# Performance work log

Measured on AMD Instinct MI355X. Metric: run time of the kernel, lower is better.

## Reference

```python
import jax, jax.numpy as jnp
import numpy as np

HEADS = 4
SCALE = 10.0
DIM = 128
VOL = (16, 16, 16)
BATCH = 2
EPS = 1e-12  # F.normalize eps


def setup_inputs() -> dict:
    key = jax.random.key(0)
    ks = jax.random.split(key, 7)
    h, w, z = VOL
    shape = (BATCH, DIM, h, w, z)
    wstd = 1.0 / np.sqrt(DIM)
    return {
        "x": jax.random.normal(ks[0], shape, dtype=jnp.float32),
        "cond_x": jax.random.normal(ks[1], shape, dtype=jnp.float32),
        "Wq": jax.random.normal(ks[2], (DIM, DIM), dtype=jnp.float32) * wstd,
        "bq": jnp.zeros((DIM,), dtype=jnp.float32),
        "Wk": jax.random.normal(ks[3], (DIM, DIM), dtype=jnp.float32) * wstd,
        "bk": jnp.zeros((DIM,), dtype=jnp.float32),
        "Wv": jax.random.normal(ks[4], (DIM, DIM), dtype=jnp.float32) * wstd,
        "bv": jnp.zeros((DIM,), dtype=jnp.float32),
        "Wo": jax.random.normal(ks[5], (DIM, DIM), dtype=jnp.float32) * wstd,
        "bo": jnp.zeros((DIM,), dtype=jnp.float32),
    }


def _l2norm_last(t):
    # F.normalize(t, dim=-1): divide by max(||t||_2, eps) along last axis
    n = jnp.sqrt(jnp.sum(t * t, axis=-1, keepdims=True))
    return t / jnp.maximum(n, EPS)


def reference(x, cond_x, Wq, bq, Wk, bk, Wv, bv, Wo, bo):
    b, c, h, w, z = x.shape
    N = h * w * z
    d = c // HEADS
    xf = x.reshape(b, c, N)          # conv1x1 == per-voxel linear over channels
    cf = cond_x.reshape(b, c, N)
    q = jnp.einsum('oc,bcn->bon', Wq, xf) + bq[None, :, None]
    k = jnp.einsum('oc,bcn->bon', Wk, cf) + bk[None, :, None]
    v = jnp.einsum('oc,bcn->bon', Wv, cf) + bv[None, :, None]
    # 'b (h c) n -> b h c n'
    q = q.reshape(b, HEADS, d, N)
    k = k.reshape(b, HEADS, d, N)
    v = v.reshape(b, HEADS, d, N)
    # NOTE: original normalizes dim=-1 of [b,h,d,N] -> over the SPATIAL axis
    q = _l2norm_last(q)
    k = _l2norm_last(k)
    sim = jnp.einsum('bhdi,bhdj->bhij', q, k) * SCALE   # [b,h,N,N]
    attn = jax.nn.softmax(sim, axis=-1)
    out = jnp.einsum('bhij,bhdj->bhid', attn, v)        # [b,h,N,d]
    # 'b h n d -> b (h d) n' then back to volume
    out = out.transpose(0, 1, 3, 2).reshape(b, c, N)
    out = jnp.einsum('oc,bcn->bon', Wo, out) + bo[None, :, None]
    return out.reshape(b, c, h, w, z)
```

## Files before the change

kernel.cpp:

```cpp
#include <hip/hip_runtime.h>
#include <hip/hip_bf16.h>
#include <math.h>

#define NSP 4096
#define CD 128
#define NB 2
#define NH 4
#define JS 4
#define JSTEP 64
#define NSTEP ((NSP / JS) / JSTEP)

typedef __attribute__((ext_vector_type(8))) short bf16x8;
typedef __attribute__((ext_vector_type(4))) float f32x4;

static constexpr float QSCALE = 10.0f * 1.4426950408889634f;

__device__ __forceinline__ ushort f2bf(float f) {
    union { float f; unsigned u; } v; v.f = f;
    unsigned r = v.u + 0x7fffu + ((v.u >> 16) & 1u);
    return (ushort)(r >> 16);
}
__device__ __forceinline__ float bf2f(ushort u) {
    union { unsigned u; float f; } v; v.u = ((unsigned)u) << 16;
    return v.f;
}
__device__ __forceinline__ unsigned pk2bf(float a, float b) {
    union { __hip_bfloat162 h; unsigned u; } t;
    t.h = __float22bfloat162_rn(make_float2(a, b));
    return t.u;
}
__device__ __forceinline__ void gload_lds16(const void* g, void* l) {
    __builtin_amdgcn_global_load_lds(
        (const __attribute__((address_space(1))) unsigned int*)g,
        (__attribute__((address_space(3))) unsigned int*)l, 16, 0, 0);
}

__global__ __launch_bounds__(256) void cast_all(
    const float* __restrict__ x, const float* __restrict__ cx,
    const float* __restrict__ Wq, const float* __restrict__ Wk,
    const float* __restrict__ Wv, const float* __restrict__ Wo,
    ushort* __restrict__ Xt, ushort* __restrict__ Ct, ushort* __restrict__ Wall)
{
    const int t = threadIdx.x;
    if (blockIdx.x >= 128) {
        const int sub = blockIdx.x - 128;
        const int m = blockIdx.z * 2 + blockIdx.y;
        const float* src = (m == 0) ? Wq : (m == 1) ? Wk : (m == 2) ? Wv : Wo;
        const int off = sub * 1024 + t * 4;
        const float4 v = *(const float4*)(src + off);
        ushort4 o;
        o.x = f2bf(v.x); o.y = f2bf(v.y); o.z = f2bf(v.z); o.w = f2bf(v.w);
        *(ushort4*)(Wall + m * 16384 + off) = o;
        return;
    }
    __shared__ ushort L[32][130];
    const int n0 = blockIdx.x * 32;
    const int b  = blockIdx.y;
    const float* in = (blockIdx.z == 0) ? x : cx;
    ushort* outp    = (blockIdx.z == 0) ? Xt : Ct;
    const int nl = t & 31, cq = t >> 5;
    #pragma unroll
    for (int cc = cq; cc < CD; cc += 8)
        L[nl][cc] = f2bf(in[((size_t)b * CD + cc) * NSP + n0 + nl]);
    __syncthreads();
    const int nr = t >> 3, cs = (t & 7) * 16;
    unsigned u[8];
    #pragma unroll
    for (int w = 0; w < 8; ++w)
        u[w] = (unsigned)L[nr][cs + 2 * w] | ((unsigned)L[nr][cs + 2 * w + 1] << 16);
    ushort* dst = outp + ((size_t)(b * NSP + n0 + nr)) * CD + cs;
    *(uint4*)(dst)     = make_uint4(u[0], u[1], u[2], u[3]);
    *(uint4*)(dst + 8) = make_uint4(u[4], u[5], u[6], u[7]);
}

__global__ __launch_bounds__(256) void proj_qkv_mfma(
    const ushort* __restrict__ Xt, const ushort* __restrict__ Ct,
    const ushort* __restrict__ Wall,
    const float* __restrict__ Bq, const float* __restrict__ Bk, const float* __restrict__ Bv,
    ushort* __restrict__ qh, ushort* __restrict__ kh, ushort* __restrict__ V16,
    float* __restrict__ partQ, float* __restrict__ partK)
{
    const int t = threadIdx.x;
    const int wid = t >> 6, lane = t & 63;
    const int g = lane >> 4, n16 = lane & 15;
    const int nt = blockIdx.x;
    const int b  = nt >> 8;
    const int xblk = nt & 255;
    const int nb = xblk * 16;
    const int o0 = (blockIdx.y * 4 + wid) * 16;

    const ushort* Wq = Wall;
    const ushort* Wk = Wall + 16384;
    const ushort* Wv = Wall + 32768;
    const size_t xrow = ((size_t)(b * NSP + nb + n16)) * CD;
    const size_t wrow = (size_t)(o0 + n16) * CD;

    f32x4 aq = {0,0,0,0}, ak = {0,0,0,0}, av = {0,0,0,0};
    #pragma unroll
    for (int ks = 0; ks < 4; ++ks) {
        const int k0 = ks * 32 + g * 8;
        const bf16x8 bx = *(const bf16x8*)(Xt + xrow + k0);
        const bf16x8 bc = *(const bf16x8*)(Ct + xrow + k0);
        const bf16x8 wqf = *(const bf16x8*)(Wq + wrow + k0);
        const bf16x8 wkf = *(const bf16x8*)(Wk + wrow + k0);
        const bf16x8 wvf = *(const bf16x8*)(Wv + wrow + k0);
        aq = __builtin_amdgcn_mfma_f32_16x16x32_bf16(wqf, bx, aq, 0, 0, 0);
        ak = __builtin_amdgcn_mfma_f32_16x16x32_bf16(wkf, bc, ak, 0, 0, 0);
        av = __builtin_amdgcn_mfma_f32_16x16x32_bf16(wvf, bc, av, 0, 0, 0);
    }
    float sq[4], sk[4];
    #pragma unroll
    for (int r = 0; r < 4; ++r) {
        const int o = o0 + 4 * g + r;
        const size_t row = ((size_t)(b * CD + o)) * NSP + nb + n16;
        const float qv = aq[r] + Bq[o];
        const float kv = ak[r] + Bk[o];
        qh[row]  = f2bf(qv);
        kh[row]  = f2bf(kv);
        V16[row] = f2bf(av[r] + Bv[o]);
        sq[r] = qv * qv; sk[r] = kv * kv;
    }
    #pragma unroll
    for (int r = 0; r < 4; ++r) {
        #pragma unroll
        for (int off = 1; off < 16; off <<= 1) {
            sq[r] += __shfl_xor(sq[r], off);
            sk[r] += __shfl_xor(sk[r], off);
        }
    }
    if (n16 == 0) {
        #pragma unroll
        for (int r = 0; r < 4; ++r) {
            const int ch = b * CD + o0 + 4 * g + r;
            partQ[(size_t)ch * 256 + xblk] = sq[r];
            partK[(size_t)ch * 256 + xblk] = sk[r];
        }
    }
}

__global__ __launch_bounds__(256) void normfin(
    const float* __restrict__ partQ, const float* __restrict__ partK,
    float* __restrict__ scq, float* __restrict__ sck)
{
    const int ch = blockIdx.x & 255, isK = blockIdx.x >> 8;
    const float* p = (isK ? partK : partQ) + (size_t)ch * 256;
    const int t = threadIdx.x;
    float v = p[t];
    #pragma unroll
    for (int off = 32; off > 0; off >>= 1) v += __shfl_down(v, off, 64);
    __shared__ float red[4];
    if ((t & 63) == 0) red[t >> 6] = v;
    __syncthreads();
    if (t == 0) {
        const float total = red[0] + red[1] + red[2] + red[3];
        const float sc = (isK ? 1.0f : QSCALE) / fmaxf(sqrtf(total), 1e-12f);
        (isK ? sck : scq)[ch] = sc;
    }
}

__global__ __launch_bounds__(256) void pack_qk(
    const ushort* __restrict__ qh, const ushort* __restrict__ kh,
    const float* __restrict__ scq, const float* __restrict__ sck,
    ushort* __restrict__ Qt, ushort* __restrict__ Kt)
{
    const int n  = blockIdx.x * 256 + threadIdx.x;
    const int bh = blockIdx.y, cq = blockIdx.z;
    const int b = bh >> 2, h = bh & 3;
    unsigned qw[4], kw[4];
    #pragma unroll
    for (int e = 0; e < 4; ++e) {
        const int dp = cq * 4 + e;
        const int gr = b * CD + h * 32 + 2 * dp;
        const float fq0 = bf2f(qh[(size_t)gr * NSP + n]) * scq[gr];
        const float fq1 = bf2f(qh[(size_t)(gr + 1) * NSP + n]) * scq[gr + 1];
        const float fk0 = bf2f(kh[(size_t)gr * NSP + n]) * sck[gr];
        const float fk1 = bf2f(kh[(size_t)(gr + 1) * NSP + n]) * sck[gr + 1];
        qw[e] = pk2bf(fq0, fq1);
        kw[e] = pk2bf(fk0, fk1);
    }
    const int jb = n >> 6, jr = n & 63;
    const size_t base = ((size_t)(bh * (NSP / 64) + jb)) * 4 + cq;
    *(uint4*)(Qt + base * 512 + jr * 8) = make_uint4(qw[0], qw[1], qw[2], qw[3]);
    *(uint4*)(Kt + base * 512 + jr * 8) = make_uint4(kw[0], kw[1], kw[2], kw[3]);
}

__global__ __launch_bounds__(256, 4) void attn_mfma(
    const ushort* __restrict__ Qt, const ushort* __restrict__ Kt,
    const ushort* __restrict__ V16,
    unsigned* __restrict__ pacc, float* __restrict__ pl)
{
    __shared__ __align__(16) ushort Kl[4][2048];
    __shared__ __align__(16) ushort Vl[4][2048];

    const int t = threadIdx.x;
    const int wid = t >> 6, lane = t & 63;
    const int g = lane >> 4, n16 = lane & 15;
    const int f = blockIdx.x;
    const int bh = f & 7, it32 = (f >> 3) & 31, js = f >> 8;
    const int b = bh >> 2, h = bh & 3;
    const int i0 = it32 * 128 + wid * 32;

    const ushort* QtB = Qt + (size_t)bh * NSP * 32;
    const ushort* KtB = Kt + (size_t)bh * NSP * 32;
    const ushort* Vb  = V16 + (size_t)(b * CD + h * 32) * NSP;

    const size_t qoff = ((size_t)(i0 >> 6) * 4 + g) * 512 + (size_t)(i0 & 63) * 8;
    const bf16x8 qf0 = *(const bf16x8*)(QtB + qoff + n16 * 8);
    const bf16x8 qf1 = *(const bf16x8*)(QtB + qoff + (16 + n16) * 8);

    f32x4 acc00 = {0,0,0,0}, acc01 = {0,0,0,0}, acc10 = {0,0,0,0}, acc11 = {0,0,0,0};
    float l0 = 0.f, l1 = 0.f;
    const f32x4 zero = {0,0,0,0};

    const int klp = lane ^ (wid * 2);
    const int vd  = wid * 8 + (lane >> 3);
    const int vsw = (lane & 7) ^ (lane >> 3);
    auto stageK = [&](int buf, int jt) {
        gload_lds16(KtB + ((size_t)(jt >> 6) * 4 + wid) * 512 + klp * 8,
                    &Kl[buf][wid * 512]);
    };
    auto stageV = [&](int buf, int jt) {
        gload_lds16(Vb + (size_t)vd * NSP + jt + vsw * 8, &Vl[buf][wid * 512]);
    };

    const int jbeg = js * (NSP / JS);
    stageK(0, jbeg);          stageV(0, jbeg);
    stageK(1, jbeg + JSTEP);  stageV(1, jbeg + JSTEP);

    for (int step = 0; step < NSTEP; ++step) {
        const int jt = jbeg + step * JSTEP;
        if (step + 2 < NSTEP) {
            stageK((step + 2) & 3, jt + 2 * JSTEP);
            stageV((step + 2) & 3, jt + 2 * JSTEP);
            asm volatile("s_waitcnt vmcnt(4)" ::: "memory");
        } else if (step + 1 < NSTEP) {
            asm volatile("s_waitcnt vmcnt(2)" ::: "memory");
        } else {
            asm volatile("s_waitcnt vmcnt(0)" ::: "memory");
        }
        __builtin_amdgcn_s_barrier();
        const int cur = step & 3;

        #pragma unroll
        for (int s = 0; s < 2; ++s) {
            const bf16x8 kf0 = *(const bf16x8*)(&Kl[cur][g * 512 + ((s * 32 + n16) ^ (g * 2)) * 8]);
            const bf16x8 kf1 = *(const bf16x8*)(&Kl[cur][g * 512 + ((s * 32 + 16 + n16) ^ (g * 2)) * 8]);
            const int c0 = ((4 * s + (g >> 1)) ^ (n16 & 7)) * 8 + (g & 1) * 4;
            const int c1 = ((4 * s + 2 + (g >> 1)) ^ (n16 & 7)) * 8 + (g & 1) * 4;
            union { uint2 u2[2]; bf16x8 v; } v0, v1;
            v0.u2[0] = *(const uint2*)(&Vl[cur][n16 * 64 + c0]);
            v0.u2[1] = *(const uint2*)(&Vl[cur][n16 * 64 + c1]);
            v1.u2[0] = *(const uint2*)(&Vl[cur][(16 + n16) * 64 + c0]);
            v1.u2[1] = *(const uint2*)(&Vl[cur][(16 + n16) * 64 + c1]);

            #pragma unroll
            for (int it = 0; it < 2; ++it) {
                const bf16x8 qf = it ? qf1 : qf0;
                f32x4 s0 = __builtin_amdgcn_mfma_f32_16x16x32_bf16(kf0, qf, zero, 0, 0, 0);
                f32x4 s1 = __builtin_amdgcn_mfma_f32_16x16x32_bf16(kf1, qf, zero, 0, 0, 0);
                const float p0 = __builtin_amdgcn_exp2f(s0.x);
                const float p1 = __builtin_amdgcn_exp2f(s0.y);
                const float p2 = __builtin_amdgcn_exp2f(s0.z);
                const float p3 = __builtin_amdgcn_exp2f(s0.w);
                const float p4 = __builtin_amdgcn_exp2f(s1.x);
                const float p5 = __builtin_amdgcn_exp2f(s1.y);
                const float p6 = __builtin_amdgcn_exp2f(s1.z);
                const float p7 = __builtin_amdgcn_exp2f(s1.w);
                const float ps = ((p0 + p1) + (p2 + p3)) + ((p4 + p5) + (p6 + p7));
                if (it) l1 += ps; else l0 += ps;
                union { unsigned u[4]; bf16x8 v; } pf;
                pf.u[0] = pk2bf(p0, p1);
                pf.u[1] = pk2bf(p2, p3);
                pf.u[2] = pk2bf(p4, p5);
                pf.u[3] = pk2bf(p6, p7);
                if (it) {
                    acc10 = __builtin_amdgcn_mfma_f32_16x16x32_bf16(v0.v, pf.v, acc10, 0, 0, 0);
                    acc11 = __builtin_amdgcn_mfma_f32_16x16x32_bf16(v1.v, pf.v, acc11, 0, 0, 0);
                } else {
                    acc00 = __builtin_amdgcn_mfma_f32_16x16x32_bf16(v0.v, pf.v, acc00, 0, 0, 0);
                    acc01 = __builtin_amdgcn_mfma_f32_16x16x32_bf16(v1.v, pf.v, acc01, 0, 0, 0);
                }
            }
        }
    }

    l0 += __shfl_xor(l0, 16); l0 += __shfl_xor(l0, 32);
    l1 += __shfl_xor(l1, 16); l1 += __shfl_xor(l1, 32);

    const size_t base = (size_t)js * 8 + bh;
    if (lane < 16) {
        pl[base * NSP + i0 + n16]      = l0;
        pl[base * NSP + i0 + 16 + n16] = l1;
    }
    unsigned* pb = pacc + base * 16 * NSP;
    const int col0 = i0 + n16, col1 = i0 + 16 + n16;
    pb[(size_t)(2 * g)     * NSP + col0] = pk2bf(acc00[0], acc00[1]);
    pb[(size_t)(2 * g + 1) * NSP + col0] = pk2bf(acc00[2], acc00[3]);
    pb[(size_t)(8 + 2 * g)     * NSP + col0] = pk2bf(acc01[0], acc01[1]);
    pb[(size_t)(8 + 2 * g + 1) * NSP + col0] = pk2bf(acc01[2], acc01[3]);
    pb[(size_t)(2 * g)     * NSP + col1] = pk2bf(acc10[0], acc10[1]);
    pb[(size_t)(2 * g + 1) * NSP + col1] = pk2bf(acc10[2], acc10[3]);
    pb[(size_t)(8 + 2 * g)     * NSP + col1] = pk2bf(acc11[0], acc11[1]);
    pb[(size_t)(8 + 2 * g + 1) * NSP + col1] = pk2bf(acc11[2], acc11[3]);
}

__global__ __launch_bounds__(256) void combine_kernel(
    const unsigned* __restrict__ pacc, const float* __restrict__ pl,
    ushort* __restrict__ Yt)
{
    const int i  = blockIdx.x * 256 + threadIdx.x;
    const int bh = blockIdx.y, z = blockIdx.z;
    const int b = bh >> 2, h = bh & 3;
    float L = 0.f;
    #pragma unroll
    for (int s = 0; s < JS; ++s) L += pl[((size_t)(s * 8 + bh)) * NSP + i];
    const float invL = 1.0f / L;
    unsigned u[4];
    #pragma unroll
    for (int e = 0; e < 4; ++e) {
        const int dp = z * 4 + e;
        float a0 = 0.f, a1 = 0.f;
        #pragma unroll
        for (int s = 0; s < JS; ++s) {
            const unsigned w = pacc[(((size_t)(s * 8 + bh)) * 16 + dp) * NSP + i];
            union { unsigned u; float f; } lo, hi;
            lo.u = w << 16; hi.u = w & 0xffff0000u;
            a0 += lo.f; a1 += hi.f;
        }
        u[e] = pk2bf(a0 * invL, a1 * invL);
    }
    ushort* dst = Yt + ((size_t)(b * NSP + i)) * CD + h * 32 + z * 8;
    *(uint4*)(dst) = make_uint4(u[0], u[1], u[2], u[3]);
}

__global__ __launch_bounds__(256) void proj_out_mfma(
    const ushort* __restrict__ Yt, const ushort* __restrict__ Wall,
    const float* __restrict__ Bo, float* __restrict__ outp)
{
    const int t = threadIdx.x;
    const int wid = t >> 6, lane = t & 63;
    const int g = lane >> 4, n16 = lane & 15;
    const int nt = blockIdx.x;
    const int b  = nt >> 8;
    const int nb = (nt & 255) * 16;
    const int o0 = (blockIdx.y * 4 + wid) * 16;

    const ushort* Wo = Wall + 49152;
    const size_t xrow = ((size_t)(b * NSP + nb + n16)) * CD;
    const size_t wrow = (size_t)(o0 + n16) * CD;

    f32x4 a = {0,0,0,0};
    #pragma unroll
    for (int ks = 0; ks < 4; ++ks) {
        const int k0 = ks * 32 + g * 8;
        const bf16x8 bx = *(const bf16x8*)(Yt + xrow + k0);
        const bf16x8 wf = *(const bf16x8*)(Wo + wrow + k0);
        a = __builtin_amdgcn_mfma_f32_16x16x32_bf16(wf, bx, a, 0, 0, 0);
    }
    #pragma unroll
    for (int r = 0; r < 4; ++r) {
        const int o = o0 + 4 * g + r;
        outp[((size_t)(b * CD + o)) * NSP + nb + n16] = a[r] + Bo[o];
    }
}

extern "C" void kernel_launch(void* const* d_in, const int* in_sizes, int n_in,
                              void* d_out, int out_size, void* d_ws, size_t ws_size,
                              hipStream_t stream)
{
    const float* x  = (const float*)d_in[0];
    const float* cx = (const float*)d_in[1];
    const float* Wq = (const float*)d_in[2];
    const float* bq = (const float*)d_in[3];
    const float* Wk = (const float*)d_in[4];
    const float* bk = (const float*)d_in[5];
    const float* Wv = (const float*)d_in[6];
    const float* bv = (const float*)d_in[7];
    const float* Wo = (const float*)d_in[8];
    const float* bo = (const float*)d_in[9];
    float* out = (float*)d_out;

    char* w = (char*)d_ws;
    ushort*  qh   = (ushort*)w;  w += (size_t)NB * CD * NSP * 2;
    ushort*  kh   = (ushort*)w;  w += (size_t)NB * CD * NSP * 2;
    float*   scq  = (float*)w;   w += 1024;
    float*   sck  = (float*)w;   w += 1024;
    float*   partQ = (float*)w;  w += (size_t)NB * CD * 256 * 4;
    float*   partK = (float*)w;  w += (size_t)NB * CD * 256 * 4;
    ushort*  Qt   = (ushort*)w;  w += (size_t)NB * NH * NSP * 32 * 2;
    ushort*  Kt   = (ushort*)w;  w += (size_t)NB * NH * NSP * 32 * 2;
    ushort*  V16  = (ushort*)w;  w += (size_t)NB * CD * NSP * 2;
    unsigned* pacc = (unsigned*)w; w += (size_t)JS * 8 * 16 * NSP * 4;
    float*   pl   = (float*)w;   w += (size_t)JS * 8 * NSP * 4;
    ushort*  Xt   = (ushort*)w;  w += (size_t)NB * NSP * CD * 2;
    ushort*  Ct   = (ushort*)w;  w += (size_t)NB * NSP * CD * 2;
    ushort*  Yt   = (ushort*)w;  w += (size_t)NB * NSP * CD * 2;
    ushort*  Wall = (ushort*)w;

    cast_all<<<dim3(144, NB, 2), 256, 0, stream>>>(x, cx, Wq, Wk, Wv, Wo, Xt, Ct, Wall);
    proj_qkv_mfma<<<dim3(512, 2), 256, 0, stream>>>(Xt, Ct, Wall, bq, bk, bv,
                                                    qh, kh, V16, partQ, partK);
    normfin<<<dim3(512), 256, 0, stream>>>(partQ, partK, scq, sck);
    pack_qk<<<dim3(16, 8, 4), 256, 0, stream>>>(qh, kh, scq, sck, Qt, Kt);
    attn_mfma<<<dim3(1024), 256, 0, stream>>>(Qt, Kt, V16, pacc, pl);
    combine_kernel<<<dim3(16, 8, 4), 256, 0, stream>>>(pacc, pl, Yt);
    proj_out_mfma<<<dim3(512, 2), 256, 0, stream>>>(Yt, Wall, bo, out);
}
```

Measured before the change: 72.90 us.

## Fold Q/K normalization into attention, drop pack kernel, fuse combine with output projection

The QKV projection now writes unnormalized Q and K straight into the tiled layout the attention kernel reads, so the separate pack_qk pass and the qh/kh intermediates go away. The Q and K norms are merged into one per-channel factor that the attention kernel applies to its Q fragments on load. The split-K combine and the output projection are fused into one kernel that stages Y in swizzled LDS instead of a global buffer. This removes two launches and several global round-trips. In exchange, Q and K are stored as scattered 2-byte writes, and Q is rounded to bf16 twice (before and after scaling), with K left unscaled in bf16.

```diff
diff --git a/kernel.cpp b/kernel.cpp
--- a/kernel.cpp
+++ b/kernel.cpp
@@ -77,7 +77,7 @@
     const ushort* __restrict__ Xt, const ushort* __restrict__ Ct,
     const ushort* __restrict__ Wall,
     const float* __restrict__ Bq, const float* __restrict__ Bk, const float* __restrict__ Bv,
-    ushort* __restrict__ qh, ushort* __restrict__ kh, ushort* __restrict__ V16,
+    ushort* __restrict__ Qt, ushort* __restrict__ Kt, ushort* __restrict__ V16,
     float* __restrict__ partQ, float* __restrict__ partK)
 {
     const int t = threadIdx.x;
@@ -108,16 +108,19 @@
         ak = __builtin_amdgcn_mfma_f32_16x16x32_bf16(wkf, bc, ak, 0, 0, 0);
         av = __builtin_amdgcn_mfma_f32_16x16x32_bf16(wvf, bc, av, 0, 0, 0);
     }
+    const int jb = nb >> 6, jr = (nb & 63) + n16;
     float sq[4], sk[4];
     #pragma unroll
     for (int r = 0; r < 4; ++r) {
         const int o = o0 + 4 * g + r;
-        const size_t row = ((size_t)(b * CD + o)) * NSP + nb + n16;
         const float qv = aq[r] + Bq[o];
         const float kv = ak[r] + Bk[o];
-        qh[row]  = f2bf(qv);
-        kh[row]  = f2bf(kv);
-        V16[row] = f2bf(av[r] + Bv[o]);
+        V16[((size_t)(b * CD + o)) * NSP + nb + n16] = f2bf(av[r] + Bv[o]);
+        const int bh = b * NH + (o >> 5);
+        const size_t idx = (((size_t)(bh * 64 + jb)) * 4 + ((o & 31) >> 3)) * 512
+                         + jr * 8 + (o & 7);
+        Qt[idx] = f2bf(qv);
+        Kt[idx] = f2bf(kv);
         sq[r] = qv * qv; sk[r] = kv * kv;
     }
     #pragma unroll
@@ -140,53 +143,30 @@
 
 __global__ __launch_bounds__(256) void normfin(
     const float* __restrict__ partQ, const float* __restrict__ partK,
-    float* __restrict__ scq, float* __restrict__ sck)
-{
-    const int ch = blockIdx.x & 255, isK = blockIdx.x >> 8;
-    const float* p = (isK ? partK : partQ) + (size_t)ch * 256;
-    const int t = threadIdx.x;
-    float v = p[t];
-    #pragma unroll
-    for (int off = 32; off > 0; off >>= 1) v += __shfl_down(v, off, 64);
-    __shared__ float red[4];
-    if ((t & 63) == 0) red[t >> 6] = v;
+    float* __restrict__ fsc)
+{
+    const int ch = blockIdx.x;
+    const int t = threadIdx.x;
+    float vq = partQ[(size_t)ch * 256 + t];
+    float vk = partK[(size_t)ch * 256 + t];
+    #pragma unroll
+    for (int off = 32; off > 0; off >>= 1) {
+        vq += __shfl_down(vq, off, 64);
+        vk += __shfl_down(vk, off, 64);
+    }
+    __shared__ float redq[4], redk[4];
+    if ((t & 63) == 0) { redq[t >> 6] = vq; redk[t >> 6] = vk; }
     __syncthreads();
     if (t == 0) {
-        const float total = red[0] + red[1] + red[2] + red[3];
-        const float sc = (isK ? 1.0f : QSCALE) / fmaxf(sqrtf(total), 1e-12f);
-        (isK ? sck : scq)[ch] = sc;
-    }
-}
-
-__global__ __launch_bounds__(256) void pack_qk(
-    const ushort* __restrict__ qh, const ushort* __restrict__ kh,
-    const float* __restrict__ scq, const float* __restrict__ sck,
-    ushort* __restrict__ Qt, ushort* __restrict__ Kt)
-{
-    const int n  = blockIdx.x * 256 + threadIdx.x;
-    const int bh = blockIdx.y, cq = blockIdx.z;
-    const int b = bh >> 2, h = bh & 3;
-    unsigned qw[4], kw[4];
-    #pragma unroll
-    for (int e = 0; e < 4; ++e) {
-        const int dp = cq * 4 + e;
-        const int gr = b * CD + h * 32 + 2 * dp;
-        const float fq0 = bf2f(qh[(size_t)gr * NSP + n]) * scq[gr];
-        const float fq1 = bf2f(qh[(size_t)(gr + 1) * NSP + n]) * scq[gr + 1];
-        const float fk0 = bf2f(kh[(size_t)gr * NSP + n]) * sck[gr];
-        const float fk1 = bf2f(kh[(size_t)(gr + 1) * NSP + n]) * sck[gr + 1];
-        qw[e] = pk2bf(fq0, fq1);
-        kw[e] = pk2bf(fk0, fk1);
-    }
-    const int jb = n >> 6, jr = n & 63;
-    const size_t base = ((size_t)(bh * (NSP / 64) + jb)) * 4 + cq;
-    *(uint4*)(Qt + base * 512 + jr * 8) = make_uint4(qw[0], qw[1], qw[2], qw[3]);
-    *(uint4*)(Kt + base * 512 + jr * 8) = make_uint4(kw[0], kw[1], kw[2], kw[3]);
+        const float nq = sqrtf(redq[0] + redq[1] + redq[2] + redq[3]);
+        const float nk = sqrtf(redk[0] + redk[1] + redk[2] + redk[3]);
+        fsc[ch] = QSCALE / (fmaxf(nq, 1e-12f) * fmaxf(nk, 1e-12f));
+    }
 }
 
 __global__ __launch_bounds__(256, 4) void attn_mfma(
     const ushort* __restrict__ Qt, const ushort* __restrict__ Kt,
-    const ushort* __restrict__ V16,
+    const ushort* __restrict__ V16, const float* __restrict__ fsc,
     unsigned* __restrict__ pacc, float* __restrict__ pl)
 {
     __shared__ __align__(16) ushort Kl[4][2048];
@@ -204,9 +184,23 @@
     const ushort* KtB = Kt + (size_t)bh * NSP * 32;
     const ushort* Vb  = V16 + (size_t)(b * CD + h * 32) * NSP;
 
+    const float* fb = fsc + b * CD + h * 32 + g * 8;
+    const f32x4 fA = *(const f32x4*)(fb);
+    const f32x4 fB = *(const f32x4*)(fb + 4);
+
     const size_t qoff = ((size_t)(i0 >> 6) * 4 + g) * 512 + (size_t)(i0 & 63) * 8;
-    const bf16x8 qf0 = *(const bf16x8*)(QtB + qoff + n16 * 8);
-    const bf16x8 qf1 = *(const bf16x8*)(QtB + qoff + (16 + n16) * 8);
+    const bf16x8 qr0 = *(const bf16x8*)(QtB + qoff + n16 * 8);
+    const bf16x8 qr1 = *(const bf16x8*)(QtB + qoff + (16 + n16) * 8);
+    auto scaleq = [&](bf16x8 q) -> bf16x8 {
+        union { unsigned u[4]; bf16x8 v; } o;
+        o.u[0] = pk2bf(bf2f((ushort)q[0]) * fA.x, bf2f((ushort)q[1]) * fA.y);
+        o.u[1] = pk2bf(bf2f((ushort)q[2]) * fA.z, bf2f((ushort)q[3]) * fA.w);
+        o.u[2] = pk2bf(bf2f((ushort)q[4]) * fB.x, bf2f((ushort)q[5]) * fB.y);
+        o.u[3] = pk2bf(bf2f((ushort)q[6]) * fB.z, bf2f((ushort)q[7]) * fB.w);
+        return o.v;
+    };
+    const bf16x8 qf0 = scaleq(qr0);
+    const bf16x8 qf1 = scaleq(qr1);
 
     f32x4 acc00 = {0,0,0,0}, acc01 = {0,0,0,0}, acc10 = {0,0,0,0}, acc11 = {0,0,0,0};
     float l0 = 0.f, l1 = 0.f;
@@ -304,63 +298,64 @@
     pb[(size_t)(8 + 2 * g + 1) * NSP + col1] = pk2bf(acc11[2], acc11[3]);
 }
 
-__global__ __launch_bounds__(256) void combine_kernel(
+__global__ __launch_bounds__(256) void combine_proj_out(
     const unsigned* __restrict__ pacc, const float* __restrict__ pl,
-    ushort* __restrict__ Yt)
-{
-    const int i  = blockIdx.x * 256 + threadIdx.x;
-    const int bh = blockIdx.y, z = blockIdx.z;
-    const int b = bh >> 2, h = bh & 3;
-    float L = 0.f;
-    #pragma unroll
-    for (int s = 0; s < JS; ++s) L += pl[((size_t)(s * 8 + bh)) * NSP + i];
-    const float invL = 1.0f / L;
-    unsigned u[4];
-    #pragma unroll
-    for (int e = 0; e < 4; ++e) {
-        const int dp = z * 4 + e;
-        float a0 = 0.f, a1 = 0.f;
-        #pragma unroll
-        for (int s = 0; s < JS; ++s) {
-            const unsigned w = pacc[(((size_t)(s * 8 + bh)) * 16 + dp) * NSP + i];
-            union { unsigned u; float f; } lo, hi;
-            lo.u = w << 16; hi.u = w & 0xffff0000u;
-            a0 += lo.f; a1 += hi.f;
-        }
-        u[e] = pk2bf(a0 * invL, a1 * invL);
-    }
-    ushort* dst = Yt + ((size_t)(b * NSP + i)) * CD + h * 32 + z * 8;
-    *(uint4*)(dst) = make_uint4(u[0], u[1], u[2], u[3]);
-}
-
-__global__ __launch_bounds__(256) void proj_out_mfma(
-    const ushort* __restrict__ Yt, const ushort* __restrict__ Wall,
-    const float* __restrict__ Bo, float* __restrict__ outp)
-{
-    const int t = threadIdx.x;
-    const int wid = t >> 6, lane = t & 63;
-    const int g = lane >> 4, n16 = lane & 15;
+    const ushort* __restrict__ Wall, const float* __restrict__ Bo,
+    float* __restrict__ outp)
+{
+    __shared__ __align__(16) ushort Yl[16][128];
+    const int t = threadIdx.x;
     const int nt = blockIdx.x;
     const int b  = nt >> 8;
     const int nb = (nt & 255) * 16;
-    const int o0 = (blockIdx.y * 4 + wid) * 16;
-
+
+    {
+        const int nl = t & 15, hh = (t >> 4) & 3, q = t >> 6;
+        const int bh = b * NH + hh;
+        const int n = nb + nl;
+        float L = 0.f;
+        #pragma unroll
+        for (int s = 0; s < JS; ++s) L += pl[((size_t)(s * 8 + bh)) * NSP + n];
+        const float invL = 1.0f / L;
+        unsigned u[4];
+        #pragma unroll
+        for (int e = 0; e < 4; ++e) {
+            const int dp = q * 4 + e;
+            float a0 = 0.f, a1 = 0.f;
+            #pragma unroll
+            for (int s = 0; s < JS; ++s) {
+                const unsigned w = pacc[(((size_t)(s * 8 + bh)) * 16 + dp) * NSP + n];
+                union { unsigned u; float f; } lo, hi;
+                lo.u = w << 16; hi.u = w & 0xffff0000u;
+                a0 += lo.f; a1 += hi.f;
+            }
+            u[e] = pk2bf(a0 * invL, a1 * invL);
+        }
+        const int chunk = hh * 4 + q;
+        *(uint4*)(&Yl[nl][((chunk ^ (nl & 7)) * 8)]) = make_uint4(u[0], u[1], u[2], u[3]);
+    }
+    __syncthreads();
+
+    const int wid = t >> 6, lane = t & 63;
+    const int g = lane >> 4, n16 = lane & 15;
     const ushort* Wo = Wall + 49152;
-    const size_t xrow = ((size_t)(b * NSP + nb + n16)) * CD;
-    const size_t wrow = (size_t)(o0 + n16) * CD;
-
-    f32x4 a = {0,0,0,0};
-    #pragma unroll
-    for (int ks = 0; ks < 4; ++ks) {
-        const int k0 = ks * 32 + g * 8;
-        const bf16x8 bx = *(const bf16x8*)(Yt + xrow + k0);
-        const bf16x8 wf = *(const bf16x8*)(Wo + wrow + k0);
-        a = __builtin_amdgcn_mfma_f32_16x16x32_bf16(wf, bx, a, 0, 0, 0);
-    }
-    #pragma unroll
-    for (int r = 0; r < 4; ++r) {
-        const int o = o0 + 4 * g + r;
-        outp[((size_t)(b * CD + o)) * NSP + nb + n16] = a[r] + Bo[o];
+    #pragma unroll
+    for (int half = 0; half < 2; ++half) {
+        const int o0 = half * 64 + wid * 16;
+        const size_t wrow = (size_t)(o0 + n16) * CD;
+        f32x4 a = {0,0,0,0};
+        #pragma unroll
+        for (int ks = 0; ks < 4; ++ks) {
+            const bf16x8 wf = *(const bf16x8*)(Wo + wrow + ks * 32 + g * 8);
+            const int chunk = ks * 4 + g;
+            const bf16x8 yf = *(const bf16x8*)(&Yl[n16][((chunk ^ (n16 & 7)) * 8)]);
+            a = __builtin_amdgcn_mfma_f32_16x16x32_bf16(wf, yf, a, 0, 0, 0);
+        }
+        #pragma unroll
+        for (int r = 0; r < 4; ++r) {
+            const int o = o0 + 4 * g + r;
+            outp[((size_t)(b * CD + o)) * NSP + nb + n16] = a[r] + Bo[o];
+        }
     }
 }
 
@@ -381,10 +376,7 @@
     float* out = (float*)d_out;
 
     char* w = (char*)d_ws;
-    ushort*  qh   = (ushort*)w;  w += (size_t)NB * CD * NSP * 2;
-    ushort*  kh   = (ushort*)w;  w += (size_t)NB * CD * NSP * 2;
-    float*   scq  = (float*)w;   w += 1024;
-    float*   sck  = (float*)w;   w += 1024;
+    float*   fsc  = (float*)w;   w += 4096;
     float*   partQ = (float*)w;  w += (size_t)NB * CD * 256 * 4;
     float*   partK = (float*)w;  w += (size_t)NB * CD * 256 * 4;
     ushort*  Qt   = (ushort*)w;  w += (size_t)NB * NH * NSP * 32 * 2;
@@ -394,15 +386,12 @@
     float*   pl   = (float*)w;   w += (size_t)JS * 8 * NSP * 4;
     ushort*  Xt   = (ushort*)w;  w += (size_t)NB * NSP * CD * 2;
     ushort*  Ct   = (ushort*)w;  w += (size_t)NB * NSP * CD * 2;
-    ushort*  Yt   = (ushort*)w;  w += (size_t)NB * NSP * CD * 2;
     ushort*  Wall = (ushort*)w;
 
     cast_all<<<dim3(144, NB, 2), 256, 0, stream>>>(x, cx, Wq, Wk, Wv, Wo, Xt, Ct, Wall);
     proj_qkv_mfma<<<dim3(512, 2), 256, 0, stream>>>(Xt, Ct, Wall, bq, bk, bv,
-                                                    qh, kh, V16, partQ, partK);
-    normfin<<<dim3(512), 256, 0, stream>>>(partQ, partK, scq, sck);
-    pack_qk<<<dim3(16, 8, 4), 256, 0, stream>>>(qh, kh, scq, sck, Qt, Kt);
-    attn_mfma<<<dim3(1024), 256, 0, stream>>>(Qt, Kt, V16, pacc, pl);
-    combine_kernel<<<dim3(16, 8, 4), 256, 0, stream>>>(pacc, pl, Yt);
-    proj_out_mfma<<<dim3(512, 2), 256, 0, stream>>>(Yt, Wall, bo, out);
-}
+                                                    Qt, Kt, V16, partQ, partK);
+    normfin<<<dim3(256), 256, 0, stream>>>(partQ, partK, fsc);
+    attn_mfma<<<dim3(1024), 256, 0, stream>>>(Qt, Kt, V16, fsc, pacc, pl);
+    combine_proj_out<<<dim3(512), 256, 0, stream>>>(pacc, pl, Wall, bo, out);
+}
```

Measured after the change: 65.98 us. -9.5%, faster.
